# Optimization experiments

Measured on AMD Instinct MI355X. Metric: run time of the kernel, lower is better.

The kernel has to match this reference:

```python
import jax, jax.numpy as jnp
import numpy as np

B, S, D, H = 2, 2048, 1024, 16
HD = D // H  # head_dim = 64

def setup_inputs() -> dict:
    key = jax.random.key(0)
    ks = jax.random.split(key, 5)
    scale = 0.02
    return {
        "x":  jax.random.normal(ks[0], (B, S, D), dtype=jnp.float32),
        "Wq": jax.random.normal(ks[1], (D, D), dtype=jnp.float32) * scale,
        "Wk": jax.random.normal(ks[2], (D, D), dtype=jnp.float32) * scale,
        "Wv": jax.random.normal(ks[3], (D, D), dtype=jnp.float32) * scale,
        "Wo": jax.random.normal(ks[4], (D, D), dtype=jnp.float32) * scale,
    }

def reference(x, Wq, Wk, Wv, Wo):
    b, s, d = x.shape
    # projections (bias-free linear): [b,s,d] @ [d,d]
    q = (x @ Wq).reshape(b, s, H, HD).transpose(0, 2, 1, 3)  # [b,h,s,hd]
    k = (x @ Wk).reshape(b, s, H, HD).transpose(0, 2, 1, 3)
    v = (x @ Wv).reshape(b, s, H, HD).transpose(0, 2, 1, 3)
    scale = jnp.asarray(1.0 / np.sqrt(HD), dtype=x.dtype)
    scores = jnp.einsum('bhqd,bhkd->bhqk', q, k) * scale  # [b,h,s,s]
    causal = jnp.tril(jnp.ones((s, s), dtype=bool))
    scores = jnp.where(causal, scores, jnp.asarray(-jnp.inf, dtype=scores.dtype))
    attn = jax.nn.softmax(scores, axis=-1)
    out = jnp.einsum('bhqk,bhkd->bhqd', attn, v)  # [b,h,s,hd]
    out = out.transpose(0, 2, 1, 3).reshape(b, s, d)
    return out @ Wo
```

## Files before the change

kernel.cpp:

```cpp
#include <hip/hip_runtime.h>
#include <hip/hip_bf16.h>
#include <cstdint>

typedef __bf16 bf16;
typedef bf16 bf16x8 __attribute__((ext_vector_type(8)));
typedef float f32x4 __attribute__((ext_vector_type(4)));

#define MFMA16(a, b, c) __builtin_amdgcn_mfma_f32_16x16x32_bf16(a, b, c, 0, 0, 0)

struct rawF { f32x4 a, b; };
__device__ inline rawF ldr(const float* p) {
  rawF r; r.a = *(const f32x4*)p; r.b = *(const f32x4*)(p + 4); return r;
}
__device__ inline bf16x8 ldr(const bf16* p) { return *(const bf16x8*)p; }
__device__ inline bf16x8 cv(const rawF& r) {
  bf16x8 o;
#pragma unroll
  for (int i = 0; i < 4; ++i) { o[i] = (bf16)r.a[i]; o[i + 4] = (bf16)r.b[i]; }
  return o;
}
__device__ inline bf16x8 cv(const bf16x8& r) { return r; }
__device__ inline void stC(bf16* C, size_t i, float v) { C[i] = (bf16)v; }
__device__ inline void stC(float* C, size_t i, float v) { C[i] = v; }

__global__ __launch_bounds__(256) void prep_wt(const float* __restrict__ W0,
                                               const float* __restrict__ W1,
                                               const float* __restrict__ W2,
                                               const float* __restrict__ W3,
                                               bf16* __restrict__ Wt, int n) {
  const float* Ws[4] = {W0, W1, W2, W3};
  const float* W = Ws[blockIdx.z];
  bf16* out = Wt + (size_t)blockIdx.z * n * n;
  __shared__ bf16 t[32][33];
  int bx = blockIdx.x * 32, by = blockIdx.y * 32;
  int tx = threadIdx.x & 31, ty = threadIdx.x >> 5;
#pragma unroll
  for (int i = 0; i < 32; i += 8)
    t[ty + i][tx] = (bf16)W[(size_t)(by + ty + i) * n + bx + tx];
  __syncthreads();
#pragma unroll
  for (int i = 0; i < 32; i += 8)
    out[(size_t)(bx + ty + i) * n + by + tx] = t[tx][ty + i];
}

__global__ __launch_bounds__(256) void vtrans(const bf16* __restrict__ V, bf16* __restrict__ Vt) {
  constexpr int Sn = 2048, Dn = 1024;
  __shared__ bf16 t[32][33];
  int s0 = blockIdx.x * 32, hd0 = blockIdx.y * 32, bh = blockIdx.z;
  int b = bh >> 4, h = bh & 15;
  int tx = threadIdx.x & 31, ty = threadIdx.x >> 5;
#pragma unroll
  for (int i = 0; i < 32; i += 8)
    t[ty + i][tx] = V[(size_t)(b * Sn + s0 + ty + i) * Dn + h * 64 + hd0 + tx];
  __syncthreads();
#pragma unroll
  for (int i = 0; i < 32; i += 8)
    Vt[(size_t)bh * 64 * Sn + (size_t)(hd0 + ty + i) * Sn + s0 + tx] = t[tx][ty + i];
}

template <typename TA, typename TC, bool BT>
__global__ __launch_bounds__(256) void gemm3(const TA* __restrict__ A,
                                             const void* __restrict__ B0p,
                                             const void* __restrict__ B1p,
                                             const void* __restrict__ B2p,
                                             TC* __restrict__ C0, TC* __restrict__ C1,
                                             TC* __restrict__ C2, int M, int N, int K, int nblk) {
  constexpr int LDA = 40;
  constexpr int LDB = BT ? 40 : 32;
  __shared__ bf16 As[128 * LDA];
  __shared__ bf16 Bs[128 * LDB];
  int tid = threadIdx.x, wave = tid >> 6, lane = tid & 63;
  int la = lane & 15, quad = lane >> 4;
  int wr = (wave >> 1) * 64, wc = (wave & 1) * 64;
  int by = blockIdx.y;
  int sel = by / nblk;
  int n0 = (by - sel * nblk) * 128;
  const void* Bp = sel == 0 ? B0p : (sel == 1 ? B1p : B2p);
  TC* C = sel == 0 ? C0 : (sel == 1 ? C1 : C2);
  const TA* Ab = A + (size_t)blockIdx.x * 128 * K;
  using TB = typename std::conditional<BT, bf16, float>::type;
  const TB* Bm = (const TB*)Bp;

  int ar[2], ac[2], br[2], bc[2];
#pragma unroll
  for (int p = 0; p < 2; ++p) {
    int li = (tid + p * 256) * 8;
    ar[p] = li >> 5; ac[p] = li & 31;
    if (BT) { br[p] = li >> 5; bc[p] = li & 31; }
    else    { br[p] = li >> 7; bc[p] = li & 127; }
  }

  f32x4 zero = {0.f, 0.f, 0.f, 0.f};
  f32x4 acc[4][4];
#pragma unroll
  for (int i = 0; i < 4; ++i)
#pragma unroll
    for (int j = 0; j < 4; ++j) acc[i][j] = zero;

  decltype(ldr((const TA*)nullptr)) pa[2];
  decltype(ldr((const TB*)nullptr)) pb[2];
#pragma unroll
  for (int p = 0; p < 2; ++p) {
    pa[p] = ldr(&Ab[(size_t)ar[p] * K + ac[p]]);
    if (BT) pb[p] = ldr(&Bm[(size_t)(n0 + br[p]) * K + bc[p]]);
    else    pb[p] = ldr(&Bm[(size_t)br[p] * N + n0 + bc[p]]);
  }

  for (int k0 = 0; k0 < K; k0 += 32) {
#pragma unroll
    for (int p = 0; p < 2; ++p) {
      *(bf16x8*)&As[ar[p] * LDA + ac[p]] = cv(pa[p]);
      if constexpr (BT) {
        *(bf16x8*)&Bs[br[p] * LDB + bc[p]] = cv(pb[p]);
      } else {
        bf16x8 v = cv(pb[p]);
        int kx = br[p] ^ (((bc[p] >> 3) & 3) << 3);
#pragma unroll
        for (int j = 0; j < 8; ++j) Bs[(bc[p] + j) * 32 + kx] = v[j];
      }
    }
    __syncthreads();
    int k1 = k0 + 32;
    if (k1 < K) {
#pragma unroll
      for (int p = 0; p < 2; ++p) {
        pa[p] = ldr(&Ab[(size_t)ar[p] * K + k1 + ac[p]]);
        if (BT) pb[p] = ldr(&Bm[(size_t)(n0 + br[p]) * K + k1 + bc[p]]);
        else    pb[p] = ldr(&Bm[(size_t)(k1 + br[p]) * N + n0 + bc[p]]);
      }
    }
    bf16x8 af[4], bfr[4];
#pragma unroll
    for (int i = 0; i < 4; ++i)
      af[i] = *(const bf16x8*)&As[(wr + i * 16 + la) * LDA + quad * 8];
#pragma unroll
    for (int j = 0; j < 4; ++j) {
      int nr = wc + j * 16 + la;
      if constexpr (BT)
        bfr[j] = *(const bf16x8*)&Bs[nr * LDB + quad * 8];
      else
        bfr[j] = *(const bf16x8*)&Bs[nr * 32 + ((quad * 8) ^ (((nr >> 3) & 3) << 3))];
    }
#pragma unroll
    for (int i = 0; i < 4; ++i)
#pragma unroll
      for (int j = 0; j < 4; ++j) acc[i][j] = MFMA16(af[i], bfr[j], acc[i][j]);
    __syncthreads();
  }
#pragma unroll
  for (int i = 0; i < 4; ++i) {
#pragma unroll
    for (int j = 0; j < 4; ++j) {
      int col = n0 + wc + j * 16 + la;
#pragma unroll
      for (int r = 0; r < 4; ++r) {
        int row = blockIdx.x * 128 + wr + i * 16 + quad * 4 + r;
        stC(C, (size_t)row * N + col, acc[i][j][r]);
      }
    }
  }
}

__global__ __launch_bounds__(256) void flash_attn(const bf16* __restrict__ Q,
                                                  const bf16* __restrict__ Kg,
                                                  const bf16* __restrict__ Vtg,
                                                  bf16* __restrict__ O) {
  constexpr int D = 1024, S = 2048;
  const int LDK = 72, LDP = 72;
  const float MASK = -3.0e4f;
  const float SCL2 = 0.18033688011112042f;
  __shared__ bf16 Ks[64 * 72];
  __shared__ bf16 Vs[64 * 72];
  __shared__ bf16 Ps[4][16 * 72];

  int bx = blockIdx.x, bh = blockIdx.y;
  int b = bh >> 4, h = bh & 15;
  int tid = threadIdx.x, wave = tid >> 6, lane = tid & 63;
  int la = lane & 15, quad = lane >> 4;
  const size_t base = (size_t)b * S * D + (size_t)h * 64;
  const bf16* Qg = Q + base;
  const bf16* Kb = Kg + base;
  const bf16* Vb = Vtg + (size_t)bh * 64 * S;
  int r0 = tid >> 3, c0 = (tid & 7) * 8;

  f32x4 zero = {0.f, 0.f, 0.f, 0.f};

#pragma unroll
  for (int seg = 0; seg < 2; ++seg) {
    int qt = seg == 0 ? 31 - bx : bx;
    int q0 = qt * 64;
    int ntiles = qt + 1;

    bf16x8 aq[2];
    {
      int qrow = q0 + wave * 16 + la;
#pragma unroll
      for (int kc = 0; kc < 2; ++kc) {
        bf16x8 t = *(const bf16x8*)&Qg[(size_t)qrow * D + kc * 32 + quad * 8];
#pragma unroll
        for (int i = 0; i < 8; ++i) t[i] = (bf16)((float)t[i] * SCL2);
        aq[kc] = t;
      }
    }

    f32x4 o[4];
#pragma unroll
    for (int nt = 0; nt < 4; ++nt) o[nt] = zero;
    float m_l = MASK, l_l = 0.f;

    bf16x8 kr0 = *(const bf16x8*)&Kb[(size_t)r0 * D + c0];
    bf16x8 kr1 = *(const bf16x8*)&Kb[(size_t)(r0 + 32) * D + c0];
    bf16x8 vr0 = *(const bf16x8*)&Vb[(size_t)r0 * S + c0];
    bf16x8 vr1 = *(const bf16x8*)&Vb[(size_t)(r0 + 32) * S + c0];

    for (int t = 0; t < ntiles; ++t) {
      int kb = t * 64;
      *(bf16x8*)&Ks[r0 * LDK + c0] = kr0;
      *(bf16x8*)&Ks[(r0 + 32) * LDK + c0] = kr1;
      *(bf16x8*)&Vs[r0 * LDK + c0] = vr0;
      *(bf16x8*)&Vs[(r0 + 32) * LDK + c0] = vr1;
      __syncthreads();
      if (t + 1 < ntiles) {
        int kb2 = kb + 64;
        kr0 = *(const bf16x8*)&Kb[(size_t)(kb2 + r0) * D + c0];
        kr1 = *(const bf16x8*)&Kb[(size_t)(kb2 + r0 + 32) * D + c0];
        vr0 = *(const bf16x8*)&Vb[(size_t)r0 * S + kb2 + c0];
        vr1 = *(const bf16x8*)&Vb[(size_t)(r0 + 32) * S + kb2 + c0];
      }

      f32x4 s[4];
#pragma unroll
      for (int nt = 0; nt < 4; ++nt) {
        bf16x8 k0f = *(const bf16x8*)&Ks[(nt * 16 + la) * LDK + quad * 8];
        bf16x8 k1f = *(const bf16x8*)&Ks[(nt * 16 + la) * LDK + 32 + quad * 8];
        f32x4 z = zero;
        z = MFMA16(k0f, aq[0], z);
        z = MFMA16(k1f, aq[1], z);
        s[nt] = z;
      }

      if (t == qt) {
        int qa = q0 + wave * 16 + la;
#pragma unroll
        for (int nt = 0; nt < 4; ++nt)
#pragma unroll
          for (int r = 0; r < 4; ++r) {
            int ka = kb + nt * 16 + quad * 4 + r;
            s[nt][r] = (ka > qa) ? MASK : s[nt][r];
          }
      }

      float mx = m_l;
#pragma unroll
      for (int nt = 0; nt < 4; ++nt)
#pragma unroll
        for (int r = 0; r < 4; ++r) mx = fmaxf(mx, s[nt][r]);
      mx = fmaxf(mx, __shfl_xor(mx, 16, 64));
      mx = fmaxf(mx, __shfl_xor(mx, 32, 64));
      float alpha = exp2f(m_l - mx);
      float rs = 0.f;
#pragma unroll
      for (int nt = 0; nt < 4; ++nt)
#pragma unroll
        for (int r = 0; r < 4; ++r) {
          float p = exp2f(s[nt][r] - mx);
          s[nt][r] = p;
          rs += p;
        }
      rs += __shfl_xor(rs, 16, 64);
      rs += __shfl_xor(rs, 32, 64);
      l_l = l_l * alpha + rs;
      m_l = mx;

#pragma unroll
      for (int nt = 0; nt < 4; ++nt)
#pragma unroll
        for (int r = 0; r < 4; ++r)
          Ps[wave][la * LDP + nt * 16 + quad * 4 + r] = (bf16)s[nt][r];

      float ab[4];
#pragma unroll
      for (int r = 0; r < 4; ++r) ab[r] = __shfl(alpha, quad * 4 + r, 64);
#pragma unroll
      for (int nt = 0; nt < 4; ++nt)
#pragma unroll
        for (int r = 0; r < 4; ++r) o[nt][r] *= ab[r];

#pragma unroll
      for (int kc = 0; kc < 2; ++kc) {
        bf16x8 ap = *(const bf16x8*)&Ps[wave][la * LDP + kc * 32 + quad * 8];
#pragma unroll
        for (int nt = 0; nt < 4; ++nt) {
          bf16x8 bv = *(const bf16x8*)&Vs[(nt * 16 + la) * LDK + kc * 32 + quad * 8];
          o[nt] = MFMA16(ap, bv, o[nt]);
        }
      }
      __syncthreads();
    }

    float inv[4];
#pragma unroll
    for (int r = 0; r < 4; ++r) {
      float lv = __shfl(l_l, quad * 4 + r, 64);
      inv[r] = (lv > 1e-30f) ? 1.0f / lv : 0.0f;
    }
#pragma unroll
    for (int nt = 0; nt < 4; ++nt) {
      int hd = nt * 16 + la;
#pragma unroll
      for (int r = 0; r < 4; ++r) {
        int row = q0 + wave * 16 + quad * 4 + r;
        O[base + (size_t)row * D + hd] = (bf16)(o[nt][r] * inv[r]);
      }
    }
  }
}

extern "C" void kernel_launch(void* const* d_in, const int* in_sizes, int n_in,
                              void* d_out, int out_size, void* d_ws, size_t ws_size,
                              hipStream_t stream) {
  constexpr int B = 2, S = 2048, D = 1024;
  constexpr int M = B * S;
  constexpr size_t WN = (size_t)D * D;
  constexpr size_t XN = (size_t)M * D;

  const float* x = (const float*)d_in[0];
  const float* Wq = (const float*)d_in[1];
  const float* Wk = (const float*)d_in[2];
  const float* Wv = (const float*)d_in[3];
  const float* Wo = (const float*)d_in[4];
  float* out = (float*)d_out;

  if (ws_size < 2 * XN * sizeof(bf16)) return;
  bf16* Qb = (bf16*)d_ws;
  bf16* Vtg = Qb + XN;
  bf16* Wt = Vtg + XN;
  bf16* Kb = (bf16*)d_out;
  bf16* Vb = Kb + XN;
  bool use_bt = ws_size >= (2 * XN + 4 * WN) * sizeof(bf16);

  dim3 gq(M / 128, 24), gf(M / 128, 8);
  if (use_bt) {
    prep_wt<<<dim3(32, 32, 4), 256, 0, stream>>>(Wq, Wk, Wv, Wo, Wt, D);
    gemm3<float, bf16, true><<<gq, 256, 0, stream>>>(x, Wt, Wt + WN, Wt + 2 * WN,
                                                     Qb, Kb, Vb, M, D, D, 8);
  } else {
    gemm3<float, bf16, false><<<gq, 256, 0, stream>>>(x, Wq, Wk, Wv, Qb, Kb, Vb, M, D, D, 8);
  }
  vtrans<<<dim3(S / 32, 2, 32), 256, 0, stream>>>(Vb, Vtg);
  flash_attn<<<dim3(16, 32), 256, 0, stream>>>(Qb, Kb, Vtg, Qb);
  if (use_bt) {
    gemm3<bf16, float, true><<<gf, 256, 0, stream>>>(Qb, Wt + 3 * WN, Wt + 3 * WN, Wt + 3 * WN,
                                                     out, out, out, M, D, D, 8);
  } else {
    gemm3<bf16, float, false><<<gf, 256, 0, stream>>>(Qb, Wo, Wo, Wo, out, out, out, M, D, D, 8);
  }
}
```

Before: 194.3 us.

## Split flash attention into one query tile per block and reuse workspace buffer

The attention kernel now launches 32 query-tile blocks per head, each handling a single causal tile, instead of 16 blocks that each process a paired long and short tile. The grid is launched longest-first so heavier blocks start early. Workspace handling changes so one scratch region holds the transposed Q/K/V weights, then the transposed V, then the transposed Wo, which is prepared in a separate late launch. The non-transposed GEMM fallback is removed, and the P-tile store to shared memory is vectorized. The intent is more block-level parallelism and occupancy in attention; the cost is losing the explicit work pairing and adding an extra small kernel launch.

```diff
diff --git a/kernel.cpp b/kernel.cpp
--- a/kernel.cpp
+++ b/kernel.cpp
@@ -3,6 +3,7 @@
 #include <cstdint>
 
 typedef __bf16 bf16;
+typedef bf16 bf16x4v __attribute__((ext_vector_type(4)));
 typedef bf16 bf16x8 __attribute__((ext_vector_type(8)));
 typedef float f32x4 __attribute__((ext_vector_type(4)));
 
@@ -26,9 +27,8 @@
 __global__ __launch_bounds__(256) void prep_wt(const float* __restrict__ W0,
                                                const float* __restrict__ W1,
                                                const float* __restrict__ W2,
-                                               const float* __restrict__ W3,
                                                bf16* __restrict__ Wt, int n) {
-  const float* Ws[4] = {W0, W1, W2, W3};
+  const float* Ws[3] = {W0, W1, W2};
   const float* W = Ws[blockIdx.z];
   bf16* out = Wt + (size_t)blockIdx.z * n * n;
   __shared__ bf16 t[32][33];
@@ -58,15 +58,15 @@
     Vt[(size_t)bh * 64 * Sn + (size_t)(hd0 + ty + i) * Sn + s0 + tx] = t[tx][ty + i];
 }
 
-template <typename TA, typename TC, bool BT>
-__global__ __launch_bounds__(256) void gemm3(const TA* __restrict__ A,
-                                             const void* __restrict__ B0p,
-                                             const void* __restrict__ B1p,
-                                             const void* __restrict__ B2p,
-                                             TC* __restrict__ C0, TC* __restrict__ C1,
-                                             TC* __restrict__ C2, int M, int N, int K, int nblk) {
-  constexpr int LDA = 40;
-  constexpr int LDB = BT ? 40 : 32;
+template <typename TA, typename TC>
+__global__ __launch_bounds__(256) void gemm_bt3(const TA* __restrict__ A,
+                                                const bf16* __restrict__ Bt0,
+                                                const bf16* __restrict__ Bt1,
+                                                const bf16* __restrict__ Bt2,
+                                                TC* __restrict__ C0, TC* __restrict__ C1,
+                                                TC* __restrict__ C2, int M, int N, int K,
+                                                int nblk) {
+  constexpr int LDA = 40, LDB = 40;
   __shared__ bf16 As[128 * LDA];
   __shared__ bf16 Bs[128 * LDB];
   int tid = threadIdx.x, wave = tid >> 6, lane = tid & 63;
@@ -75,19 +75,15 @@
   int by = blockIdx.y;
   int sel = by / nblk;
   int n0 = (by - sel * nblk) * 128;
-  const void* Bp = sel == 0 ? B0p : (sel == 1 ? B1p : B2p);
+  const bf16* Bm = sel == 0 ? Bt0 : (sel == 1 ? Bt1 : Bt2);
   TC* C = sel == 0 ? C0 : (sel == 1 ? C1 : C2);
   const TA* Ab = A + (size_t)blockIdx.x * 128 * K;
-  using TB = typename std::conditional<BT, bf16, float>::type;
-  const TB* Bm = (const TB*)Bp;
-
-  int ar[2], ac[2], br[2], bc[2];
+
+  int ar[2], ac[2];
 #pragma unroll
   for (int p = 0; p < 2; ++p) {
     int li = (tid + p * 256) * 8;
     ar[p] = li >> 5; ac[p] = li & 31;
-    if (BT) { br[p] = li >> 5; bc[p] = li & 31; }
-    else    { br[p] = li >> 7; bc[p] = li & 127; }
   }
 
   f32x4 zero = {0.f, 0.f, 0.f, 0.f};
@@ -98,26 +94,18 @@
     for (int j = 0; j < 4; ++j) acc[i][j] = zero;
 
   decltype(ldr((const TA*)nullptr)) pa[2];
-  decltype(ldr((const TB*)nullptr)) pb[2];
+  bf16x8 pb[2];
 #pragma unroll
   for (int p = 0; p < 2; ++p) {
     pa[p] = ldr(&Ab[(size_t)ar[p] * K + ac[p]]);
-    if (BT) pb[p] = ldr(&Bm[(size_t)(n0 + br[p]) * K + bc[p]]);
-    else    pb[p] = ldr(&Bm[(size_t)br[p] * N + n0 + bc[p]]);
+    pb[p] = ldr(&Bm[(size_t)(n0 + ar[p]) * K + ac[p]]);
   }
 
   for (int k0 = 0; k0 < K; k0 += 32) {
 #pragma unroll
     for (int p = 0; p < 2; ++p) {
       *(bf16x8*)&As[ar[p] * LDA + ac[p]] = cv(pa[p]);
-      if constexpr (BT) {
-        *(bf16x8*)&Bs[br[p] * LDB + bc[p]] = cv(pb[p]);
-      } else {
-        bf16x8 v = cv(pb[p]);
-        int kx = br[p] ^ (((bc[p] >> 3) & 3) << 3);
-#pragma unroll
-        for (int j = 0; j < 8; ++j) Bs[(bc[p] + j) * 32 + kx] = v[j];
-      }
+      *(bf16x8*)&Bs[ar[p] * LDB + ac[p]] = pb[p];
     }
     __syncthreads();
     int k1 = k0 + 32;
@@ -125,8 +113,7 @@
 #pragma unroll
       for (int p = 0; p < 2; ++p) {
         pa[p] = ldr(&Ab[(size_t)ar[p] * K + k1 + ac[p]]);
-        if (BT) pb[p] = ldr(&Bm[(size_t)(n0 + br[p]) * K + k1 + bc[p]]);
-        else    pb[p] = ldr(&Bm[(size_t)(k1 + br[p]) * N + n0 + bc[p]]);
+        pb[p] = ldr(&Bm[(size_t)(n0 + ar[p]) * K + k1 + ac[p]]);
       }
     }
     bf16x8 af[4], bfr[4];
@@ -134,13 +121,8 @@
     for (int i = 0; i < 4; ++i)
       af[i] = *(const bf16x8*)&As[(wr + i * 16 + la) * LDA + quad * 8];
 #pragma unroll
-    for (int j = 0; j < 4; ++j) {
-      int nr = wc + j * 16 + la;
-      if constexpr (BT)
-        bfr[j] = *(const bf16x8*)&Bs[nr * LDB + quad * 8];
-      else
-        bfr[j] = *(const bf16x8*)&Bs[nr * 32 + ((quad * 8) ^ (((nr >> 3) & 3) << 3))];
-    }
+    for (int j = 0; j < 4; ++j)
+      bfr[j] = *(const bf16x8*)&Bs[(wc + j * 16 + la) * LDB + quad * 8];
 #pragma unroll
     for (int i = 0; i < 4; ++i)
 #pragma unroll
@@ -173,10 +155,12 @@
   __shared__ bf16 Vs[64 * 72];
   __shared__ bf16 Ps[4][16 * 72];
 
-  int bx = blockIdx.x, bh = blockIdx.y;
+  int qt = 31 - blockIdx.x;
+  int bh = blockIdx.y;
   int b = bh >> 4, h = bh & 15;
   int tid = threadIdx.x, wave = tid >> 6, lane = tid & 63;
   int la = lane & 15, quad = lane >> 4;
+  int q0 = qt * 64;
   const size_t base = (size_t)b * S * D + (size_t)h * 64;
   const bf16* Qg = Q + base;
   const bf16* Kb = Kg + base;
@@ -185,133 +169,129 @@
 
   f32x4 zero = {0.f, 0.f, 0.f, 0.f};
 
-#pragma unroll
-  for (int seg = 0; seg < 2; ++seg) {
-    int qt = seg == 0 ? 31 - bx : bx;
-    int q0 = qt * 64;
-    int ntiles = qt + 1;
-
-    bf16x8 aq[2];
-    {
-      int qrow = q0 + wave * 16 + la;
-#pragma unroll
-      for (int kc = 0; kc < 2; ++kc) {
-        bf16x8 t = *(const bf16x8*)&Qg[(size_t)qrow * D + kc * 32 + quad * 8];
-#pragma unroll
-        for (int i = 0; i < 8; ++i) t[i] = (bf16)((float)t[i] * SCL2);
-        aq[kc] = t;
+  bf16x8 aq[2];
+  {
+    int qrow = q0 + wave * 16 + la;
+#pragma unroll
+    for (int kc = 0; kc < 2; ++kc) {
+      bf16x8 t = *(const bf16x8*)&Qg[(size_t)qrow * D + kc * 32 + quad * 8];
+#pragma unroll
+      for (int i = 0; i < 8; ++i) t[i] = (bf16)((float)t[i] * SCL2);
+      aq[kc] = t;
+    }
+  }
+
+  f32x4 o[4];
+#pragma unroll
+  for (int nt = 0; nt < 4; ++nt) o[nt] = zero;
+  float m_l = MASK, l_l = 0.f;
+
+  bf16x8 kr0 = *(const bf16x8*)&Kb[(size_t)r0 * D + c0];
+  bf16x8 kr1 = *(const bf16x8*)&Kb[(size_t)(r0 + 32) * D + c0];
+  bf16x8 vr0 = *(const bf16x8*)&Vb[(size_t)r0 * S + c0];
+  bf16x8 vr1 = *(const bf16x8*)&Vb[(size_t)(r0 + 32) * S + c0];
+
+  int ntiles = qt + 1;
+  for (int t = 0; t < ntiles; ++t) {
+    int kb = t * 64;
+    *(bf16x8*)&Ks[r0 * LDK + c0] = kr0;
+    *(bf16x8*)&Ks[(r0 + 32) * LDK + c0] = kr1;
+    *(bf16x8*)&Vs[r0 * LDK + c0] = vr0;
+    *(bf16x8*)&Vs[(r0 + 32) * LDK + c0] = vr1;
+    __syncthreads();
+    if (t + 1 < ntiles) {
+      int kb2 = kb + 64;
+      kr0 = *(const bf16x8*)&Kb[(size_t)(kb2 + r0) * D + c0];
+      kr1 = *(const bf16x8*)&Kb[(size_t)(kb2 + r0 + 32) * D + c0];
+      vr0 = *(const bf16x8*)&Vb[(size_t)r0 * S + kb2 + c0];
+      vr1 = *(const bf16x8*)&Vb[(size_t)(r0 + 32) * S + kb2 + c0];
+    }
+
+    f32x4 s[4];
+#pragma unroll
+    for (int nt = 0; nt < 4; ++nt) {
+      bf16x8 k0f = *(const bf16x8*)&Ks[(nt * 16 + la) * LDK + quad * 8];
+      bf16x8 k1f = *(const bf16x8*)&Ks[(nt * 16 + la) * LDK + 32 + quad * 8];
+      f32x4 z = zero;
+      z = MFMA16(k0f, aq[0], z);
+      z = MFMA16(k1f, aq[1], z);
+      s[nt] = z;
+    }
+
+    if (t == qt) {
+      int qa = q0 + wave * 16 + la;
+#pragma unroll
+      for (int nt = 0; nt < 4; ++nt)
+#pragma unroll
+        for (int r = 0; r < 4; ++r) {
+          int ka = kb + nt * 16 + quad * 4 + r;
+          s[nt][r] = (ka > qa) ? MASK : s[nt][r];
+        }
+    }
+
+    float mx = m_l;
+#pragma unroll
+    for (int nt = 0; nt < 4; ++nt)
+#pragma unroll
+      for (int r = 0; r < 4; ++r) mx = fmaxf(mx, s[nt][r]);
+    mx = fmaxf(mx, __shfl_xor(mx, 16, 64));
+    mx = fmaxf(mx, __shfl_xor(mx, 32, 64));
+    float alpha = exp2f(m_l - mx);
+    float rs = 0.f;
+#pragma unroll
+    for (int nt = 0; nt < 4; ++nt)
+#pragma unroll
+      for (int r = 0; r < 4; ++r) {
+        float p = exp2f(s[nt][r] - mx);
+        s[nt][r] = p;
+        rs += p;
       }
-    }
-
-    f32x4 o[4];
-#pragma unroll
-    for (int nt = 0; nt < 4; ++nt) o[nt] = zero;
-    float m_l = MASK, l_l = 0.f;
-
-    bf16x8 kr0 = *(const bf16x8*)&Kb[(size_t)r0 * D + c0];
-    bf16x8 kr1 = *(const bf16x8*)&Kb[(size_t)(r0 + 32) * D + c0];
-    bf16x8 vr0 = *(const bf16x8*)&Vb[(size_t)r0 * S + c0];
-    bf16x8 vr1 = *(const bf16x8*)&Vb[(size_t)(r0 + 32) * S + c0];
-
-    for (int t = 0; t < ntiles; ++t) {
-      int kb = t * 64;
-      *(bf16x8*)&Ks[r0 * LDK + c0] = kr0;
-      *(bf16x8*)&Ks[(r0 + 32) * LDK + c0] = kr1;
-      *(bf16x8*)&Vs[r0 * LDK + c0] = vr0;
-      *(bf16x8*)&Vs[(r0 + 32) * LDK + c0] = vr1;
-      __syncthreads();
-      if (t + 1 < ntiles) {
-        int kb2 = kb + 64;
-        kr0 = *(const bf16x8*)&Kb[(size_t)(kb2 + r0) * D + c0];
-        kr1 = *(const bf16x8*)&Kb[(size_t)(kb2 + r0 + 32) * D + c0];
-        vr0 = *(const bf16x8*)&Vb[(size_t)r0 * S + kb2 + c0];
-        vr1 = *(const bf16x8*)&Vb[(size_t)(r0 + 32) * S + kb2 + c0];
+    rs += __shfl_xor(rs, 16, 64);
+    rs += __shfl_xor(rs, 32, 64);
+    l_l = l_l * alpha + rs;
+    m_l = mx;
+
+#pragma unroll
+    for (int nt = 0; nt < 4; ++nt) {
+      bf16x4v pk;
+#pragma unroll
+      for (int r = 0; r < 4; ++r) pk[r] = (bf16)s[nt][r];
+      *(bf16x4v*)&Ps[wave][la * LDP + nt * 16 + quad * 4] = pk;
+    }
+
+    float ab[4];
+#pragma unroll
+    for (int r = 0; r < 4; ++r) ab[r] = __shfl(alpha, quad * 4 + r, 64);
+#pragma unroll
+    for (int nt = 0; nt < 4; ++nt)
+#pragma unroll
+      for (int r = 0; r < 4; ++r) o[nt][r] *= ab[r];
+
+#pragma unroll
+    for (int kc = 0; kc < 2; ++kc) {
+      bf16x8 ap = *(const bf16x8*)&Ps[wave][la * LDP + kc * 32 + quad * 8];
+#pragma unroll
+      for (int nt = 0; nt < 4; ++nt) {
+        bf16x8 bv = *(const bf16x8*)&Vs[(nt * 16 + la) * LDK + kc * 32 + quad * 8];
+        o[nt] = MFMA16(ap, bv, o[nt]);
       }
-
-      f32x4 s[4];
-#pragma unroll
-      for (int nt = 0; nt < 4; ++nt) {
-        bf16x8 k0f = *(const bf16x8*)&Ks[(nt * 16 + la) * LDK + quad * 8];
-        bf16x8 k1f = *(const bf16x8*)&Ks[(nt * 16 + la) * LDK + 32 + quad * 8];
-        f32x4 z = zero;
-        z = MFMA16(k0f, aq[0], z);
-        z = MFMA16(k1f, aq[1], z);
-        s[nt] = z;
-      }
-
-      if (t == qt) {
-        int qa = q0 + wave * 16 + la;
-#pragma unroll
-        for (int nt = 0; nt < 4; ++nt)
-#pragma unroll
-          for (int r = 0; r < 4; ++r) {
-            int ka = kb + nt * 16 + quad * 4 + r;
-            s[nt][r] = (ka > qa) ? MASK : s[nt][r];
-          }
-      }
-
-      float mx = m_l;
-#pragma unroll
-      for (int nt = 0; nt < 4; ++nt)
-#pragma unroll
-        for (int r = 0; r < 4; ++r) mx = fmaxf(mx, s[nt][r]);
-      mx = fmaxf(mx, __shfl_xor(mx, 16, 64));
-      mx = fmaxf(mx, __shfl_xor(mx, 32, 64));
-      float alpha = exp2f(m_l - mx);
-      float rs = 0.f;
-#pragma unroll
-      for (int nt = 0; nt < 4; ++nt)
-#pragma unroll
-        for (int r = 0; r < 4; ++r) {
-          float p = exp2f(s[nt][r] - mx);
-          s[nt][r] = p;
-          rs += p;
-        }
-      rs += __shfl_xor(rs, 16, 64);
-      rs += __shfl_xor(rs, 32, 64);
-      l_l = l_l * alpha + rs;
-      m_l = mx;
-
-#pragma unroll
-      for (int nt = 0; nt < 4; ++nt)
-#pragma unroll
-        for (int r = 0; r < 4; ++r)
-          Ps[wave][la * LDP + nt * 16 + quad * 4 + r] = (bf16)s[nt][r];
-
-      float ab[4];
-#pragma unroll
-      for (int r = 0; r < 4; ++r) ab[r] = __shfl(alpha, quad * 4 + r, 64);
-#pragma unroll
-      for (int nt = 0; nt < 4; ++nt)
-#pragma unroll
-        for (int r = 0; r < 4; ++r) o[nt][r] *= ab[r];
-
-#pragma unroll
-      for (int kc = 0; kc < 2; ++kc) {
-        bf16x8 ap = *(const bf16x8*)&Ps[wave][la * LDP + kc * 32 + quad * 8];
-#pragma unroll
-        for (int nt = 0; nt < 4; ++nt) {
-          bf16x8 bv = *(const bf16x8*)&Vs[(nt * 16 + la) * LDK + kc * 32 + quad * 8];
-          o[nt] = MFMA16(ap, bv, o[nt]);
-        }
-      }
-      __syncthreads();
-    }
-
-    float inv[4];
+    }
+    __syncthreads();
+  }
+
+  float inv[4];
+#pragma unroll
+  for (int r = 0; r < 4; ++r) {
+    float lv = __shfl(l_l, quad * 4 + r, 64);
+    inv[r] = (lv > 1e-30f) ? 1.0f / lv : 0.0f;
+  }
+#pragma unroll
+  for (int nt = 0; nt < 4; ++nt) {
+    int hd = nt * 16 + la;
 #pragma unroll
     for (int r = 0; r < 4; ++r) {
-      float lv = __shfl(l_l, quad * 4 + r, 64);
-      inv[r] = (lv > 1e-30f) ? 1.0f / lv : 0.0f;
-    }
-#pragma unroll
-    for (int nt = 0; nt < 4; ++nt) {
-      int hd = nt * 16 + la;
-#pragma unroll
-      for (int r = 0; r < 4; ++r) {
-        int row = q0 + wave * 16 + quad * 4 + r;
-        O[base + (size_t)row * D + hd] = (bf16)(o[nt][r] * inv[r]);
-      }
+      int row = q0 + wave * 16 + quad * 4 + r;
+      O[base + (size_t)row * D + hd] = (bf16)(o[nt][r] * inv[r]);
     }
   }
 }
@@ -333,26 +313,16 @@
 
   if (ws_size < 2 * XN * sizeof(bf16)) return;
   bf16* Qb = (bf16*)d_ws;
-  bf16* Vtg = Qb + XN;
-  bf16* Wt = Vtg + XN;
+  bf16* R2 = Qb + XN;
   bf16* Kb = (bf16*)d_out;
   bf16* Vb = Kb + XN;
-  bool use_bt = ws_size >= (2 * XN + 4 * WN) * sizeof(bf16);
-
-  dim3 gq(M / 128, 24), gf(M / 128, 8);
-  if (use_bt) {
-    prep_wt<<<dim3(32, 32, 4), 256, 0, stream>>>(Wq, Wk, Wv, Wo, Wt, D);
-    gemm3<float, bf16, true><<<gq, 256, 0, stream>>>(x, Wt, Wt + WN, Wt + 2 * WN,
-                                                     Qb, Kb, Vb, M, D, D, 8);
-  } else {
-    gemm3<float, bf16, false><<<gq, 256, 0, stream>>>(x, Wq, Wk, Wv, Qb, Kb, Vb, M, D, D, 8);
-  }
-  vtrans<<<dim3(S / 32, 2, 32), 256, 0, stream>>>(Vb, Vtg);
-  flash_attn<<<dim3(16, 32), 256, 0, stream>>>(Qb, Kb, Vtg, Qb);
-  if (use_bt) {
-    gemm3<bf16, float, true><<<gf, 256, 0, stream>>>(Qb, Wt + 3 * WN, Wt + 3 * WN, Wt + 3 * WN,
-                                                     out, out, out, M, D, D, 8);
-  } else {
-    gemm3<bf16, float, false><<<gf, 256, 0, stream>>>(Qb, Wo, Wo, Wo, out, out, out, M, D, D, 8);
-  }
-}
+
+  prep_wt<<<dim3(32, 32, 3), 256, 0, stream>>>(Wq, Wk, Wv, R2, D);
+  gemm_bt3<float, bf16><<<dim3(M / 128, 24), 256, 0, stream>>>(
+      x, R2, R2 + WN, R2 + 2 * WN, Qb, Kb, Vb, M, D, D, 8);
+  vtrans<<<dim3(S / 32, 2, 32), 256, 0, stream>>>(Vb, R2);
+  flash_attn<<<dim3(32, 32), 256, 0, stream>>>(Qb, Kb, R2, Qb);
+  prep_wt<<<dim3(32, 32, 1), 256, 0, stream>>>(Wo, Wo, Wo, R2, D);
+  gemm_bt3<bf16, float><<<dim3(M / 128, 8), 256, 0, stream>>>(
+      Qb, R2, R2, R2, out, out, out, M, D, D, 8);
+}
```

Measured after the change: 231.4 us. +19.1%, slower.
